# Performance work log

Measured on AMD Instinct MI355X. Metric: run time of the kernel, lower is better.

Reference implementation:

```python
import jax, jax.numpy as jnp
import numpy as np


def _rgcn(x, src, dst, et, basis, comp, root, bias):
    # Basis-decomposed RGCNConv (PyG semantics): per-relation mean aggregation
    # over incoming edges + root transform + bias.
    N = x.shape[0]
    R = comp.shape[0]
    W = jnp.einsum('rb,bio->rio', comp, basis)          # [R, in, out]
    xr = jnp.einsum('ni,rio->rno', x, W)                 # [R, N, out]
    msg = xr[et, src]                                    # [E, out] gather per edge
    seg = dst * R + et                                   # (target, relation) segment id
    cnt = jax.ops.segment_sum(jnp.ones(et.shape, x.dtype), seg, num_segments=N * R)
    norm = 1.0 / jnp.maximum(cnt, 1.0)                   # mean per (dst, relation)
    msg = msg * norm[seg][:, None]
    agg = jax.ops.segment_sum(msg, dst, num_segments=N)  # scatter-add to targets
    return agg + x @ root + bias


def setup_inputs() -> dict:
    key = jax.random.key(0)
    ks = jax.random.split(key, 20)
    N, E, R, B, F, D, C, NB = 100000, 1600000, 5, 512, 4, 32, 5, 2
    s = 0.1
    inp = {
        'x': jax.random.normal(ks[0], (N, F), jnp.float32),
        'edge_index': jax.random.randint(ks[1], (2, E), 0, N, dtype=jnp.int32),
        'edge_type': jax.random.randint(ks[2], (E,), 0, R, dtype=jnp.int32),
        'start_nodes': jax.random.randint(ks[3], (B,), 0, N, dtype=jnp.int32),
        # layer 0: in=F, out=D
        'basis0': jax.random.normal(ks[4], (NB, F, D), jnp.float32) * s,
        'comp0': jax.random.normal(ks[5], (R, NB), jnp.float32) * s,
        'root0': jax.random.normal(ks[6], (F, D), jnp.float32) * s,
        'bias0': jax.random.normal(ks[7], (D,), jnp.float32) * s,
        # layers 1..3: in=out=D, stacked
        'basis': jax.random.normal(ks[8], (3, NB, D, D), jnp.float32) * s,
        'comp': jax.random.normal(ks[9], (3, R, NB), jnp.float32) * s,
        'root': jax.random.normal(ks[10], (3, D, D), jnp.float32) * s,
        'bias': jax.random.normal(ks[11], (3, D), jnp.float32) * s,
        # MLP head: sum(latent_dim)=128 -> 128 -> C
        'lin1_w': jax.random.normal(ks[12], (4 * D, 128), jnp.float32) * s,
        'lin1_b': jax.random.normal(ks[13], (128,), jnp.float32) * s,
        'lin2_w': jax.random.normal(ks[14], (128, C), jnp.float32) * s,
        'lin2_b': jax.random.normal(ks[15], (C,), jnp.float32) * s,
    }
    return inp


def reference(x, edge_index, edge_type, start_nodes, basis0, comp0, root0, bias0,
              basis, comp, root, bias, lin1_w, lin1_b, lin2_w, lin2_b):
    src, dst = edge_index[0], edge_index[1]
    h = jnp.tanh(_rgcn(x, src, dst, edge_type, basis0, comp0, root0, bias0))
    states = [h]
    for l in range(basis.shape[0]):
        h = jnp.tanh(_rgcn(h, src, dst, edge_type, basis[l], comp[l], root[l], bias[l]))
        states.append(h)
    concat = jnp.concatenate(states, axis=1)             # [N, 128]
    # Per-graph readout: the walk's degenerate n_walks=1 branch, i.e. the
    # start (user) node's concatenated state (sequential backtracking walk
    # replaced by its deterministic initialization path; eval mode, no dropout).
    acc = concat[start_nodes]                            # [B, 128]
    h1 = jax.nn.relu(acc @ lin1_w + lin1_b)
    logits = h1 @ lin2_w + lin2_b
    return jax.nn.log_softmax(logits, axis=-1)
```

## Files before the change

kernel.cpp:

```cpp
#include <hip/hip_runtime.h>
#include <cstdint>

#define N_NODES 100000
#define N_EDGES 1600000
#define R_REL   5
#define NBASIS  2
#define B_START 512
#define PART_SZ 12500
#define NBUCK   256
#define BUCK_SZ 391
#define EPB     6250
#define STAGE_CAP 7000

__device__ __forceinline__ unsigned short f2bf(float f) {
    unsigned u = __float_as_uint(f);
    unsigned r = (u + 0x7FFF + ((u >> 16) & 1)) >> 16;
    return (unsigned short)r;
}


__global__ __launch_bounds__(256) void k_cntb(
    const int* __restrict__ ei, int* __restrict__ bhist) {
    __shared__ int lh[NBUCK];
    int tid = threadIdx.x;
    lh[tid] = 0;
    __syncthreads();
    int base = blockIdx.x * EPB;
    for (int j = tid; j < EPB; j += 256) {
        int dst = ei[N_EDGES + base + j];
        atomicAdd(&lh[dst / BUCK_SZ], 1);
    }
    __syncthreads();
    bhist[blockIdx.x * NBUCK + tid] = lh[tid];
}

__global__ __launch_bounds__(256) void k_scanb(
    int* __restrict__ bhist, int* __restrict__ bbase) {
    int b = threadIdx.x;
    int tot = 0;
    for (int i = 0; i < NBUCK; i += 8) {
        int v0 = bhist[(i + 0) * NBUCK + b], v1 = bhist[(i + 1) * NBUCK + b];
        int v2 = bhist[(i + 2) * NBUCK + b], v3 = bhist[(i + 3) * NBUCK + b];
        int v4 = bhist[(i + 4) * NBUCK + b], v5 = bhist[(i + 5) * NBUCK + b];
        int v6 = bhist[(i + 6) * NBUCK + b], v7 = bhist[(i + 7) * NBUCK + b];
        tot += v0 + v1 + v2 + v3 + v4 + v5 + v6 + v7;
    }
    __shared__ int s[NBUCK];
    s[b] = tot;
    __syncthreads();
    for (int o = 1; o < NBUCK; o <<= 1) {
        int v = (b >= o) ? s[b - o] : 0;
        __syncthreads();
        s[b] += v;
        __syncthreads();
    }
    int base = s[b] - tot;
    bbase[b] = base;
    if (b == NBUCK - 1) bbase[NBUCK] = s[NBUCK - 1];
    int run = base;
    for (int i = 0; i < NBUCK; i += 8) {
        int v0 = bhist[(i + 0) * NBUCK + b], v1 = bhist[(i + 1) * NBUCK + b];
        int v2 = bhist[(i + 2) * NBUCK + b], v3 = bhist[(i + 3) * NBUCK + b];
        int v4 = bhist[(i + 4) * NBUCK + b], v5 = bhist[(i + 5) * NBUCK + b];
        int v6 = bhist[(i + 6) * NBUCK + b], v7 = bhist[(i + 7) * NBUCK + b];
        bhist[(i + 0) * NBUCK + b] = run; run += v0;
        bhist[(i + 1) * NBUCK + b] = run; run += v1;
        bhist[(i + 2) * NBUCK + b] = run; run += v2;
        bhist[(i + 3) * NBUCK + b] = run; run += v3;
        bhist[(i + 4) * NBUCK + b] = run; run += v4;
        bhist[(i + 5) * NBUCK + b] = run; run += v5;
        bhist[(i + 6) * NBUCK + b] = run; run += v6;
        bhist[(i + 7) * NBUCK + b] = run; run += v7;
    }
}

__global__ __launch_bounds__(256) void k_scat(
    const int* __restrict__ ei, const int* __restrict__ et,
    const int* __restrict__ bhist, int* __restrict__ arena) {
    __shared__ int lc[NBUCK];
    int tid = threadIdx.x;
    lc[tid] = bhist[blockIdx.x * NBUCK + tid];
    __syncthreads();
    int base = blockIdx.x * EPB;
    for (int j = tid; j < EPB; j += 256) {
        int e   = base + j;
        int src = ei[e];
        int dst = ei[N_EDGES + e];
        int t   = et[e];
        int bk  = dst / BUCK_SZ;
        int dl  = dst - bk * BUCK_SZ;
        int pos = atomicAdd(&lc[bk], 1);
        arena[pos] = src | (t << 17) | (dl << 20);
    }
}

__global__ __launch_bounds__(256) void k_build(
    const int* __restrict__ arena, const int* __restrict__ bbase,
    int* __restrict__ off, int* __restrict__ pk_m, float* __restrict__ pk_nv) {
    __shared__ int deg5[BUCK_SZ * R_REL];
    __shared__ int loff[BUCK_SZ + 1];
    __shared__ int cur[BUCK_SZ];
    __shared__ int stg[STAGE_CAP];
    int b = blockIdx.x, tid = threadIdx.x;
    int base = bbase[b], end = bbase[b + 1];
    int count = end - base;
    for (int i = tid; i < BUCK_SZ * R_REL; i += 256) deg5[i] = 0;
    __syncthreads();
    for (int i = tid; i < count; i += 256) {
        int r  = arena[base + i];
        int dl = ((unsigned)r) >> 20;
        int t  = (r >> 17) & 7;
        atomicAdd(&deg5[dl * R_REL + t], 1);
    }
    __syncthreads();
    if (tid == 0) {
        int run = 0;
        for (int dl = 0; dl < BUCK_SZ; dl++) {
            loff[dl] = run;
            run += deg5[dl * R_REL + 0] + deg5[dl * R_REL + 1] +
                   deg5[dl * R_REL + 2] + deg5[dl * R_REL + 3] +
                   deg5[dl * R_REL + 4];
        }
        loff[BUCK_SZ] = run;
    }
    __syncthreads();
    for (int dl = tid; dl < BUCK_SZ; dl += 256) {
        int n = b * BUCK_SZ + dl;
        if (n < N_NODES) off[n] = base + loff[dl];
        cur[dl] = loff[dl];
    }
    if (b == NBUCK - 1 && tid == 0) off[N_NODES] = N_EDGES;
    __syncthreads();
    for (int i = tid; i < count; i += 256) {
        int r  = arena[base + i];
        int dl = ((unsigned)r) >> 20;
        int rk = atomicAdd(&cur[dl], 1);
        if (rk < STAGE_CAP) stg[rk] = r;
    }
    __syncthreads();
    for (int i = tid; i < count; i += 256) {
        int r   = stg[i < STAGE_CAP ? i : STAGE_CAP - 1];
        int src = r & 0x1FFFF;
        int t   = (r >> 17) & 7;
        int dl  = ((unsigned)r) >> 20;
        int c   = deg5[dl * R_REL + t];
        pk_m[base + i]  = src | (t << 17);
        pk_nv[base + i] = 1.0f / (float)(c > 0 ? c : 1);
    }
}


template <int IN>
__global__ __launch_bounds__(256) void k_xform(
    const float* __restrict__ h_in, float* __restrict__ h_io,
    unsigned short* __restrict__ y5, const float* __restrict__ basis,
    const float* __restrict__ root, const float* __restrict__ biasL,
    const float* __restrict__ compL) {
    int tid  = threadIdx.x;
    int lane = tid & 31;
    int sub  = tid >> 5;
    int g    = blockIdx.x * 8 + sub;
    float w0[IN], w1[IN], wr[IN];
#pragma unroll
    for (int i = 0; i < IN; i++) {
        w0[i] = basis[i * 32 + lane];
        w1[i] = basis[IN * 32 + i * 32 + lane];
        wr[i] = root[i * 32 + lane];
    }
    float c0[R_REL], c1[R_REL];
#pragma unroll
    for (int r = 0; r < R_REL; r++) {
        c0[r] = compL[r * NBASIS + 0];
        c1[r] = compL[r * NBASIS + 1];
    }
    float bv = biasL[lane];
    for (int n = g; n < N_NODES; n += 8192) {
        float hn = (lane < IN) ? h_in[n * IN + lane] : 0.f;
        float a0 = 0.f, a1 = 0.f, ar = bv;
#pragma unroll
        for (int i = 0; i < IN; i++) {
            float v = __shfl(hn, i, 32);
            a0 += v * w0[i];
            a1 += v * w1[i];
            ar += v * wr[i];
        }
#pragma unroll
        for (int r = 0; r < R_REL; r++)
            y5[(size_t)r * N_NODES * 32 + n * 32 + lane] = f2bf(c0[r] * a0 + c1[r] * a1);
        h_io[n * 32 + lane] = ar;
    }
}


__global__ __launch_bounds__(256) void k_edge(
    const unsigned short* __restrict__ y5, float* __restrict__ h,
    const int* __restrict__ pk_m, const float* __restrict__ pk_nv,
    const int* __restrict__ off) {
    int tid  = threadIdx.x;
    int lane = tid & 31;
    int sub  = tid >> 5;
    int part  = blockIdx.x & 7;
    int local = (blockIdx.x >> 3) * 8 + sub;
    if (local >= PART_SZ) return;
    int n = part * PART_SZ + local;

    int hl = lane & 15;
    int eo = lane >> 4;
    float acc0 = 0.f, acc1 = 0.f;
    const unsigned* __restrict__ y32 = (const unsigned*)y5;
    int e0 = off[n], e1 = off[n + 1];
    for (int base = e0; base < e1; base += 32) {
        int idx = base + lane;
        bool vld = idx < e1;
        int   m  = vld ? pk_m[idx] : 0;
        float nv = vld ? pk_nv[idx] : 0.f;
        int kmax = e1 - base;
        if (kmax > 32) kmax = 32;
        int kk = (kmax + 15) & ~15;
        for (int j = 0; j < kk; j += 16) {
            unsigned uu[8];
            float    vv[8];
#pragma unroll
            for (int q = 0; q < 8; q++) {
                int es = j + q * 2 + eo;
                int mq = __shfl(m, es, 32);
                vv[q]  = __shfl(nv, es, 32);
                unsigned row = ((unsigned)mq >> 17) * N_NODES + (mq & 0x1FFFF);
                uu[q] = y32[(size_t)row * 16 + hl];
            }
#pragma unroll
            for (int q = 0; q < 8; q++) {
                acc0 += vv[q] * __uint_as_float(uu[q] << 16);
                acc1 += vv[q] * __uint_as_float(uu[q] & 0xFFFF0000u);
            }
        }
    }
    acc0 += __shfl_xor(acc0, 16, 32);
    acc1 += __shfl_xor(acc1, 16, 32);
    if (eo == 0) {
        float2* h2 = (float2*)h;
        float2 hb = h2[(size_t)n * 16 + hl];
        float2 o;
        o.x = tanhf(hb.x + acc0);
        o.y = tanhf(hb.y + acc1);
        h2[(size_t)n * 16 + hl] = o;
    }
}


__global__ void k_save(const float* __restrict__ h, const int* __restrict__ start,
                       float* __restrict__ sav) {
    int t = blockIdx.x * blockDim.x + threadIdx.x;
    if (t < B_START * 32) {
        int b = t >> 5, ln = t & 31;
        sav[t] = h[start[b] * 32 + ln];
    }
}

__global__ __launch_bounds__(128) void k_mlp(
    const float* __restrict__ sav, const float* __restrict__ w1,
    const float* __restrict__ b1, const float* __restrict__ w2,
    const float* __restrict__ b2, float* __restrict__ out) {
    __shared__ float cvec[128];
    __shared__ float hb[128];
    __shared__ float lg[8];
    int b = blockIdx.x, t = threadIdx.x;
    cvec[t] = sav[(t >> 5) * (B_START * 32) + b * 32 + (t & 31)];
    __syncthreads();
    float a = b1[t];
#pragma unroll 8
    for (int k = 0; k < 128; k++) a += cvec[k] * w1[k * 128 + t];
    hb[t] = fmaxf(a, 0.f);
    __syncthreads();
    if (t < 5) {
        float a2 = b2[t];
        for (int k = 0; k < 128; k++) a2 += hb[k] * w2[k * 5 + t];
        lg[t] = a2;
    }
    __syncthreads();
    if (t < 5) {
        float m = lg[0];
        for (int j = 1; j < 5; j++) m = fmaxf(m, lg[j]);
        float s = 0.f;
        for (int j = 0; j < 5; j++) s += expf(lg[j] - m);
        out[b * 5 + t] = lg[t] - m - logf(s);
    }
}


extern "C" void kernel_launch(void* const* d_in, const int* in_sizes, int n_in,
                              void* d_out, int out_size, void* d_ws, size_t ws_size,
                              hipStream_t stream) {
    const float* x      = (const float*)d_in[0];
    const int*   ei     = (const int*)d_in[1];
    const int*   etype  = (const int*)d_in[2];
    const int*   start  = (const int*)d_in[3];
    const float* basis0 = (const float*)d_in[4];
    const float* comp0  = (const float*)d_in[5];
    const float* root0  = (const float*)d_in[6];
    const float* bias0  = (const float*)d_in[7];
    const float* basis  = (const float*)d_in[8];
    const float* comp   = (const float*)d_in[9];
    const float* root   = (const float*)d_in[10];
    const float* bias   = (const float*)d_in[11];
    const float* w1     = (const float*)d_in[12];
    const float* b1     = (const float*)d_in[13];
    const float* w2     = (const float*)d_in[14];
    const float* b2     = (const float*)d_in[15];
    float* out = (float*)d_out;

    char* p = (char*)d_ws;
    auto alloc = [&](size_t bytes) -> void* {
        void* r = (void*)p;
        p += (bytes + 255) & ~(size_t)255;
        return r;
    };
    int*            bhist = (int*)alloc((size_t)NBUCK * NBUCK * 4);
    int*            bbase = (int*)alloc((NBUCK + 1) * 4);
    int*            arena = (int*)alloc((size_t)N_EDGES * 4);
    int*            off   = (int*)alloc((N_NODES + 1) * 4);
    int*            pk_m  = (int*)alloc((size_t)N_EDGES * 4);
    float*          pk_nv = (float*)alloc((size_t)N_EDGES * 4);
    float*          h     = (float*)alloc((size_t)N_NODES * 32 * 4);
    unsigned short* y5    = (unsigned short*)alloc((size_t)R_REL * N_NODES * 32 * 2);
    float*          sav   = (float*)alloc(4 * B_START * 32 * 4);

    k_cntb<<<NBUCK, 256, 0, stream>>>(ei, bhist);
    k_scanb<<<1, 256, 0, stream>>>(bhist, bbase);
    k_scat<<<NBUCK, 256, 0, stream>>>(ei, etype, bhist, arena);
    k_build<<<NBUCK, 256, 0, stream>>>(arena, bbase, off, pk_m, pk_nv);

    int nbEdge = 8 * ((PART_SZ + 7) / 8);
    k_xform<4><<<1024, 256, 0, stream>>>(x, h, y5, basis0, root0, bias0, comp0);
    k_edge<<<nbEdge, 256, 0, stream>>>(y5, h, pk_m, pk_nv, off);
    k_save<<<64, 256, 0, stream>>>(h, start, sav);
    for (int l = 0; l < 3; l++) {
        k_xform<32><<<1024, 256, 0, stream>>>(h, h, y5,
                                              basis + (size_t)l * 2048,
                                              root + (size_t)l * 1024,
                                              bias + l * 32,
                                              comp + l * 10);
        k_edge<<<nbEdge, 256, 0, stream>>>(y5, h, pk_m, pk_nv, off);
        k_save<<<64, 256, 0, stream>>>(h, start, sav + (l + 1) * 16384);
    }

    k_mlp<<<B_START, 128, 0, stream>>>(sav, w1, b1, w2, b2, out);
}
```

Before: 399.5 us.

## Parallelize CSR scans, store per-node relation norms, widen edge gathers to 8 bytes

The single-block bucket scan becomes a parallel per-column scan plus a small scan of bucket totals, and the serial per-bucket offset loop in the build kernel becomes a block-wide parallel scan. The per-edge normalization array is replaced by a per-node, per-relation table of five floats. The edge kernel looks up the norm by edge type and reads 8-byte bf16 chunks with four edges in flight per warp. This cuts per-edge memory traffic and serial setup work, at the cost of an extra launch, a select chain in the inner loop, and an extra reduction stage.

```diff
diff --git a/kernel.cpp b/kernel.cpp
--- a/kernel.cpp
+++ b/kernel.cpp
@@ -34,52 +34,47 @@
     bhist[blockIdx.x * NBUCK + tid] = lh[tid];
 }
 
-__global__ __launch_bounds__(256) void k_scanb(
-    int* __restrict__ bhist, int* __restrict__ bbase) {
-    int b = threadIdx.x;
-    int tot = 0;
-    for (int i = 0; i < NBUCK; i += 8) {
-        int v0 = bhist[(i + 0) * NBUCK + b], v1 = bhist[(i + 1) * NBUCK + b];
-        int v2 = bhist[(i + 2) * NBUCK + b], v3 = bhist[(i + 3) * NBUCK + b];
-        int v4 = bhist[(i + 4) * NBUCK + b], v5 = bhist[(i + 5) * NBUCK + b];
-        int v6 = bhist[(i + 6) * NBUCK + b], v7 = bhist[(i + 7) * NBUCK + b];
-        tot += v0 + v1 + v2 + v3 + v4 + v5 + v6 + v7;
-    }
-    __shared__ int s[NBUCK];
-    s[b] = tot;
-    __syncthreads();
-    for (int o = 1; o < NBUCK; o <<= 1) {
-        int v = (b >= o) ? s[b - o] : 0;
-        __syncthreads();
-        s[b] += v;
-        __syncthreads();
-    }
-    int base = s[b] - tot;
-    bbase[b] = base;
-    if (b == NBUCK - 1) bbase[NBUCK] = s[NBUCK - 1];
-    int run = base;
-    for (int i = 0; i < NBUCK; i += 8) {
-        int v0 = bhist[(i + 0) * NBUCK + b], v1 = bhist[(i + 1) * NBUCK + b];
-        int v2 = bhist[(i + 2) * NBUCK + b], v3 = bhist[(i + 3) * NBUCK + b];
-        int v4 = bhist[(i + 4) * NBUCK + b], v5 = bhist[(i + 5) * NBUCK + b];
-        int v6 = bhist[(i + 6) * NBUCK + b], v7 = bhist[(i + 7) * NBUCK + b];
-        bhist[(i + 0) * NBUCK + b] = run; run += v0;
-        bhist[(i + 1) * NBUCK + b] = run; run += v1;
-        bhist[(i + 2) * NBUCK + b] = run; run += v2;
-        bhist[(i + 3) * NBUCK + b] = run; run += v3;
-        bhist[(i + 4) * NBUCK + b] = run; run += v4;
-        bhist[(i + 5) * NBUCK + b] = run; run += v5;
-        bhist[(i + 6) * NBUCK + b] = run; run += v6;
-        bhist[(i + 7) * NBUCK + b] = run; run += v7;
-    }
+__global__ __launch_bounds__(256) void k_colscan(
+    int* __restrict__ bhist, int* __restrict__ colsum) {
+    __shared__ int s[256];
+    int b = blockIdx.x, i = threadIdx.x;
+    int v = bhist[i * NBUCK + b];
+    s[i] = v;
+    __syncthreads();
+    for (int o = 1; o < 256; o <<= 1) {
+        int t = (i >= o) ? s[i - o] : 0;
+        __syncthreads();
+        s[i] += t;
+        __syncthreads();
+    }
+    bhist[i * NBUCK + b] = s[i] - v;
+    if (i == 255) colsum[b] = s[255];
+}
+
+__global__ __launch_bounds__(256) void k_tiny(
+    const int* __restrict__ colsum, int* __restrict__ bbase) {
+    __shared__ int s[256];
+    int i = threadIdx.x;
+    int v = colsum[i];
+    s[i] = v;
+    __syncthreads();
+    for (int o = 1; o < 256; o <<= 1) {
+        int t = (i >= o) ? s[i - o] : 0;
+        __syncthreads();
+        s[i] += t;
+        __syncthreads();
+    }
+    bbase[i] = s[i] - v;
+    if (i == 255) bbase[NBUCK] = s[255];
 }
 
 __global__ __launch_bounds__(256) void k_scat(
     const int* __restrict__ ei, const int* __restrict__ et,
-    const int* __restrict__ bhist, int* __restrict__ arena) {
+    const int* __restrict__ bhist, const int* __restrict__ bbase,
+    int* __restrict__ arena) {
     __shared__ int lc[NBUCK];
     int tid = threadIdx.x;
-    lc[tid] = bhist[blockIdx.x * NBUCK + tid];
+    lc[tid] = bhist[blockIdx.x * NBUCK + tid] + bbase[tid];
     __syncthreads();
     int base = blockIdx.x * EPB;
     for (int j = tid; j < EPB; j += 256) {
@@ -96,11 +91,12 @@
 
 __global__ __launch_bounds__(256) void k_build(
     const int* __restrict__ arena, const int* __restrict__ bbase,
-    int* __restrict__ off, int* __restrict__ pk_m, float* __restrict__ pk_nv) {
+    int* __restrict__ off, int* __restrict__ pk_m, float* __restrict__ nv5) {
     __shared__ int deg5[BUCK_SZ * R_REL];
     __shared__ int loff[BUCK_SZ + 1];
     __shared__ int cur[BUCK_SZ];
     __shared__ int stg[STAGE_CAP];
+    __shared__ int tsum[256];
     int b = blockIdx.x, tid = threadIdx.x;
     int base = bbase[b], end = bbase[b + 1];
     int count = end - base;
@@ -113,20 +109,37 @@
         atomicAdd(&deg5[dl * R_REL + t], 1);
     }
     __syncthreads();
-    if (tid == 0) {
-        int run = 0;
-        for (int dl = 0; dl < BUCK_SZ; dl++) {
-            loff[dl] = run;
-            run += deg5[dl * R_REL + 0] + deg5[dl * R_REL + 1] +
+    for (int dl = tid; dl < BUCK_SZ; dl += 256) {
+        loff[dl] = deg5[dl * R_REL + 0] + deg5[dl * R_REL + 1] +
                    deg5[dl * R_REL + 2] + deg5[dl * R_REL + 3] +
                    deg5[dl * R_REL + 4];
+    }
+    __syncthreads();
+    int d0 = 2 * tid, d1 = 2 * tid + 1;
+    int va = (d0 < BUCK_SZ) ? loff[d0] : 0;
+    int vb = (d1 < BUCK_SZ) ? loff[d1] : 0;
+    tsum[tid] = va + vb;
+    __syncthreads();
+    for (int o = 1; o < 256; o <<= 1) {
+        int v = (tid >= o) ? tsum[tid - o] : 0;
+        __syncthreads();
+        tsum[tid] += v;
+        __syncthreads();
+    }
+    int pre = tsum[tid] - (va + vb);
+    if (d0 < BUCK_SZ) loff[d0] = pre;
+    if (d1 < BUCK_SZ) loff[d1] = pre + va;
+    __syncthreads();
+    for (int dl = tid; dl < BUCK_SZ; dl += 256) {
+        int nn = b * BUCK_SZ + dl;
+        if (nn < N_NODES) {
+            off[nn] = base + loff[dl];
+#pragma unroll
+            for (int t = 0; t < R_REL; t++) {
+                int c = deg5[dl * R_REL + t];
+                nv5[nn * R_REL + t] = 1.0f / (float)(c > 0 ? c : 1);
+            }
         }
-        loff[BUCK_SZ] = run;
-    }
-    __syncthreads();
-    for (int dl = tid; dl < BUCK_SZ; dl += 256) {
-        int n = b * BUCK_SZ + dl;
-        if (n < N_NODES) off[n] = base + loff[dl];
         cur[dl] = loff[dl];
     }
     if (b == NBUCK - 1 && tid == 0) off[N_NODES] = N_EDGES;
@@ -139,13 +152,8 @@
     }
     __syncthreads();
     for (int i = tid; i < count; i += 256) {
-        int r   = stg[i < STAGE_CAP ? i : STAGE_CAP - 1];
-        int src = r & 0x1FFFF;
-        int t   = (r >> 17) & 7;
-        int dl  = ((unsigned)r) >> 20;
-        int c   = deg5[dl * R_REL + t];
-        pk_m[base + i]  = src | (t << 17);
-        pk_nv[base + i] = 1.0f / (float)(c > 0 ? c : 1);
+        int r = stg[i < STAGE_CAP ? i : STAGE_CAP - 1];
+        pk_m[base + i] = r & 0xFFFFF;
     }
 }
 
@@ -194,7 +202,7 @@
 
 __global__ __launch_bounds__(256) void k_edge(
     const unsigned short* __restrict__ y5, float* __restrict__ h,
-    const int* __restrict__ pk_m, const float* __restrict__ pk_nv,
+    const int* __restrict__ pk_m, const float* __restrict__ nv5,
     const int* __restrict__ off) {
     int tid  = threadIdx.x;
     int lane = tid & 31;
@@ -204,46 +212,72 @@
     if (local >= PART_SZ) return;
     int n = part * PART_SZ + local;
 
-    int hl = lane & 15;
-    int eo = lane >> 4;
-    float acc0 = 0.f, acc1 = 0.f;
-    const unsigned* __restrict__ y32 = (const unsigned*)y5;
+    int slot = lane >> 3;
+    int cpos = lane & 7;
+    float nvt0 = nv5[n * R_REL + 0];
+    float nvt1 = nv5[n * R_REL + 1];
+    float nvt2 = nv5[n * R_REL + 2];
+    float nvt3 = nv5[n * R_REL + 3];
+    float nvt4 = nv5[n * R_REL + 4];
+
+    float a0 = 0.f, a1 = 0.f, a2 = 0.f, a3 = 0.f;
+    const uint2* __restrict__ yv = (const uint2*)y5;
     int e0 = off[n], e1 = off[n + 1];
     for (int base = e0; base < e1; base += 32) {
-        int idx = base + lane;
-        bool vld = idx < e1;
-        int   m  = vld ? pk_m[idx] : 0;
-        float nv = vld ? pk_nv[idx] : 0.f;
+        int idx  = base + lane;
+        int m    = (idx < e1) ? pk_m[idx] : 0;
         int kmax = e1 - base;
         if (kmax > 32) kmax = 32;
-        int kk = (kmax + 15) & ~15;
-        for (int j = 0; j < kk; j += 16) {
-            unsigned uu[8];
-            float    vv[8];
-#pragma unroll
-            for (int q = 0; q < 8; q++) {
-                int es = j + q * 2 + eo;
-                int mq = __shfl(m, es, 32);
-                vv[q]  = __shfl(nv, es, 32);
-                unsigned row = ((unsigned)mq >> 17) * N_NODES + (mq & 0x1FFFF);
-                uu[q] = y32[(size_t)row * 16 + hl];
+        int j = 0;
+        for (; j + 16 <= kmax; j += 16) {
+            uint2 uu[4];
+            float vv[4];
+#pragma unroll
+            for (int q = 0; q < 4; q++) {
+                int mq = __shfl(m, j + q * 4 + slot, 32);
+                int et = mq >> 17;
+                vv[q] = (et == 0) ? nvt0 : (et == 1) ? nvt1 : (et == 2) ? nvt2
+                      : (et == 3) ? nvt3 : nvt4;
+                unsigned row = (unsigned)et * N_NODES + (mq & 0x1FFFF);
+                uu[q] = yv[(size_t)row * 8 + cpos];
             }
 #pragma unroll
-            for (int q = 0; q < 8; q++) {
-                acc0 += vv[q] * __uint_as_float(uu[q] << 16);
-                acc1 += vv[q] * __uint_as_float(uu[q] & 0xFFFF0000u);
+            for (int q = 0; q < 4; q++) {
+                float v = vv[q];
+                a0 += v * __uint_as_float(uu[q].x << 16);
+                a1 += v * __uint_as_float(uu[q].x & 0xFFFF0000u);
+                a2 += v * __uint_as_float(uu[q].y << 16);
+                a3 += v * __uint_as_float(uu[q].y & 0xFFFF0000u);
             }
         }
-    }
-    acc0 += __shfl_xor(acc0, 16, 32);
-    acc1 += __shfl_xor(acc1, 16, 32);
-    if (eo == 0) {
-        float2* h2 = (float2*)h;
-        float2 hb = h2[(size_t)n * 16 + hl];
-        float2 o;
-        o.x = tanhf(hb.x + acc0);
-        o.y = tanhf(hb.y + acc1);
-        h2[(size_t)n * 16 + hl] = o;
+        for (; j < kmax; j += 4) {
+            int es = j + slot;
+            int mq = __shfl(m, es, 32);
+            int et = mq >> 17;
+            float v = (et == 0) ? nvt0 : (et == 1) ? nvt1 : (et == 2) ? nvt2
+                    : (et == 3) ? nvt3 : nvt4;
+            v = (es < kmax) ? v : 0.f;
+            unsigned row = (unsigned)et * N_NODES + (mq & 0x1FFFF);
+            uint2 u = yv[(size_t)row * 8 + cpos];
+            a0 += v * __uint_as_float(u.x << 16);
+            a1 += v * __uint_as_float(u.x & 0xFFFF0000u);
+            a2 += v * __uint_as_float(u.y << 16);
+            a3 += v * __uint_as_float(u.y & 0xFFFF0000u);
+        }
+    }
+    a0 += __shfl_xor(a0, 8, 32);  a0 += __shfl_xor(a0, 16, 32);
+    a1 += __shfl_xor(a1, 8, 32);  a1 += __shfl_xor(a1, 16, 32);
+    a2 += __shfl_xor(a2, 8, 32);  a2 += __shfl_xor(a2, 16, 32);
+    a3 += __shfl_xor(a3, 8, 32);  a3 += __shfl_xor(a3, 16, 32);
+    if (lane < 8) {
+        float4* h4 = (float4*)h;
+        float4 hb = h4[(size_t)n * 8 + cpos];
+        float4 o;
+        o.x = tanhf(hb.x + a0);
+        o.y = tanhf(hb.y + a1);
+        o.z = tanhf(hb.z + a2);
+        o.w = tanhf(hb.w + a3);
+        h4[(size_t)n * 8 + cpos] = o;
     }
 }
 
@@ -315,24 +349,26 @@
         p += (bytes + 255) & ~(size_t)255;
         return r;
     };
-    int*            bhist = (int*)alloc((size_t)NBUCK * NBUCK * 4);
-    int*            bbase = (int*)alloc((NBUCK + 1) * 4);
-    int*            arena = (int*)alloc((size_t)N_EDGES * 4);
-    int*            off   = (int*)alloc((N_NODES + 1) * 4);
-    int*            pk_m  = (int*)alloc((size_t)N_EDGES * 4);
-    float*          pk_nv = (float*)alloc((size_t)N_EDGES * 4);
-    float*          h     = (float*)alloc((size_t)N_NODES * 32 * 4);
-    unsigned short* y5    = (unsigned short*)alloc((size_t)R_REL * N_NODES * 32 * 2);
-    float*          sav   = (float*)alloc(4 * B_START * 32 * 4);
+    int*            bhist  = (int*)alloc((size_t)NBUCK * NBUCK * 4);
+    int*            colsum = (int*)alloc(NBUCK * 4);
+    int*            bbase  = (int*)alloc((NBUCK + 1) * 4);
+    int*            arena  = (int*)alloc((size_t)N_EDGES * 4);
+    int*            off    = (int*)alloc((N_NODES + 1) * 4);
+    int*            pk_m   = (int*)alloc((size_t)N_EDGES * 4);
+    float*          nv5    = (float*)alloc((size_t)N_NODES * R_REL * 4);
+    float*          h      = (float*)alloc((size_t)N_NODES * 32 * 4);
+    unsigned short* y5     = (unsigned short*)alloc((size_t)R_REL * N_NODES * 32 * 2);
+    float*          sav    = (float*)alloc(4 * B_START * 32 * 4);
 
     k_cntb<<<NBUCK, 256, 0, stream>>>(ei, bhist);
-    k_scanb<<<1, 256, 0, stream>>>(bhist, bbase);
-    k_scat<<<NBUCK, 256, 0, stream>>>(ei, etype, bhist, arena);
-    k_build<<<NBUCK, 256, 0, stream>>>(arena, bbase, off, pk_m, pk_nv);
+    k_colscan<<<NBUCK, 256, 0, stream>>>(bhist, colsum);
+    k_tiny<<<1, 256, 0, stream>>>(colsum, bbase);
+    k_scat<<<NBUCK, 256, 0, stream>>>(ei, etype, bhist, bbase, arena);
+    k_build<<<NBUCK, 256, 0, stream>>>(arena, bbase, off, pk_m, nv5);
 
     int nbEdge = 8 * ((PART_SZ + 7) / 8);
     k_xform<4><<<1024, 256, 0, stream>>>(x, h, y5, basis0, root0, bias0, comp0);
-    k_edge<<<nbEdge, 256, 0, stream>>>(y5, h, pk_m, pk_nv, off);
+    k_edge<<<nbEdge, 256, 0, stream>>>(y5, h, pk_m, nv5, off);
     k_save<<<64, 256, 0, stream>>>(h, start, sav);
     for (int l = 0; l < 3; l++) {
         k_xform<32><<<1024, 256, 0, stream>>>(h, h, y5,
@@ -340,7 +376,7 @@
                                               root + (size_t)l * 1024,
                                               bias + l * 32,
                                               comp + l * 10);
-        k_edge<<<nbEdge, 256, 0, stream>>>(y5, h, pk_m, pk_nv, off);
+        k_edge<<<nbEdge, 256, 0, stream>>>(y5, h, pk_m, nv5, off);
         k_save<<<64, 256, 0, stream>>>(h, start, sav + (l + 1) * 16384);
     }
 
```

New measurement: 400.0 us. Within noise of the previous version (+0.1%).
